# Optimization experiments

Measured on AMD Instinct MI355X. Metric: run time of the kernel, lower is better.

## Reference

```python
import jax, jax.numpy as jnp
import numpy as np

B, K, D, C = 8192, 16, 1024, 512


def setup_inputs() -> dict:
    key = jax.random.key(0)
    k1, k2, k3, k4, k5 = jax.random.split(key, 5)
    concepts = jax.random.normal(k1, (B, K, D), dtype=jnp.float32)
    slot_ids = jax.random.randint(k2, (B,), 0, K)
    labels = jax.random.randint(k3, (B,), 0, C)
    # per-slot Linear(concept_dim -> num_classes): weight (K, C, D), bias (K, C)
    W = jax.random.normal(k4, (K, C, D), dtype=jnp.float32) / np.sqrt(D).astype(np.float32)
    bias = jax.random.normal(k5, (K, C), dtype=jnp.float32) * 0.01
    return {"concepts": concepts, "slot_ids": slot_ids, "labels": labels, "W": W, "bias": bias}


def reference(concepts, slot_ids, labels, W, bias):
    # Each example b uses slot s=slot_ids[b]: logits = concepts[b, s, :] @ W[s].T + bias[s].
    # Vectorized as K batched GEMMs over the slot axis, then gather the relevant row.
    logits = jnp.einsum('bkd,kcd->bkc', concepts, W) + bias  # (B, K, C)
    logp = jax.nn.log_softmax(logits, axis=-1)
    bidx = jnp.arange(concepts.shape[0])
    ce = -logp[bidx, slot_ids, labels]  # per-example cross entropy (B,)
    nK = W.shape[0]
    counts = jax.ops.segment_sum(jnp.ones_like(ce), slot_ids, num_segments=nK)
    sums = jax.ops.segment_sum(ce, slot_ids, num_segments=nK)
    means = sums / jnp.maximum(counts, 1.0)          # per-slot mean CE (= F.cross_entropy per group)
    present = counts > 0
    n_present = jnp.maximum(jnp.sum(present), 1)     # torch: count of unique slots, max(count,1)
    return jnp.sum(jnp.where(present, means, 0.0)) / n_present
```

## Files before the change

### kernel.cpp

```cpp
#include <hip/hip_runtime.h>
#include <hip/hip_bf16.h>

#define B_N 8192
#define K_N 16
#define D_N 1024
#define C_N 512
#define BM  16
#define CONVW_BLOCKS ((K_N * C_N * D_N) / (256 * 8))
#define GEMM_BLOCKS  (B_N / BM + K_N)

typedef __bf16 bf16x8 __attribute__((ext_vector_type(8)));
typedef float  f32x4  __attribute__((ext_vector_type(4)));
typedef unsigned int u32x4 __attribute__((ext_vector_type(4)));

static __device__ __forceinline__ unsigned short f2bf(float f) {
    union { float f; unsigned int u; } x; x.f = f;
    unsigned int r = x.u + 0x7FFFu + ((x.u >> 16) & 1u);
    return (unsigned short)(r >> 16);
}

static __device__ __forceinline__ bf16x8 load_bf8(const unsigned short* p) {
    union { u32x4 u; bf16x8 v; } t;
    t.u = *(const u32x4*)p;
    return t.v;
}

static __device__ __forceinline__ bf16x8 zero_bf8() {
    union { u32x4 u; bf16x8 v; } t;
    u32x4 z = {0u, 0u, 0u, 0u};
    t.u = z;
    return t.v;
}

__global__ __launch_bounds__(256) void setup(
        const float* __restrict__ W, unsigned short* __restrict__ Wb,
        const int* __restrict__ slot_ids, const int* __restrict__ labels,
        int* __restrict__ counts, int* __restrict__ offsets_g,
        int* __restrict__ blk_base, int* __restrict__ done,
        float* __restrict__ ce_sums, int* __restrict__ order_rows,
        int* __restrict__ lab_g) {
    __shared__ int h[256][K_N];
    __shared__ int soff[K_N];
    int t = threadIdx.x;

    if (blockIdx.x < CONVW_BLOCKS) {
        size_t i = ((size_t)blockIdx.x * 256 + t) * 8;
        f32x4 a = *(const f32x4*)(W + i);
        f32x4 b = *(const f32x4*)(W + i + 4);
        u32x4 o;
        o[0] = (unsigned)f2bf(a[0]) | ((unsigned)f2bf(a[1]) << 16);
        o[1] = (unsigned)f2bf(a[2]) | ((unsigned)f2bf(a[3]) << 16);
        o[2] = (unsigned)f2bf(b[0]) | ((unsigned)f2bf(b[1]) << 16);
        o[3] = (unsigned)f2bf(b[2]) | ((unsigned)f2bf(b[3]) << 16);
        *(u32x4*)(Wb + i) = o;
        return;
    }

    int ids[32];
    int own[K_N];

#pragma unroll
    for (int s = 0; s < K_N; ++s) h[t][s] = 0;
#pragma unroll
    for (int i = 0; i < 32; ++i) {
        int b = i * 256 + t;
        int s = slot_ids[b];
        ids[i] = s;
        h[t][s]++;
    }
#pragma unroll
    for (int s = 0; s < K_N; ++s) own[s] = h[t][s];
    __syncthreads();

    for (int d = 1; d < 256; d <<= 1) {
        int v[K_N];
        if (t >= d) {
#pragma unroll
            for (int s = 0; s < K_N; ++s) v[s] = h[t - d][s];
        }
        __syncthreads();
        if (t >= d) {
#pragma unroll
            for (int s = 0; s < K_N; ++s) h[t][s] += v[s];
        }
        __syncthreads();
    }

    if (t == 0) {
        int a = 0, nb = 0;
        blk_base[0] = 0;
#pragma unroll
        for (int s = 0; s < K_N; ++s) {
            int c = h[255][s];
            counts[s] = c;
            soff[s] = a;
            offsets_g[s] = a;
            a += c;
            nb += (c + BM - 1) / BM;
            blk_base[s + 1] = nb;
        }
        *done = 0;
    }
    if (t < K_N) ce_sums[t] = 0.f;
    __syncthreads();

#pragma unroll
    for (int s = 0; s < K_N; ++s) own[s] = soff[s] + h[t][s] - own[s];

#pragma unroll
    for (int i = 0; i < 32; ++i) {
        int b = i * 256 + t;
        int s = ids[i];
        int idx = own[s]++;
        order_rows[idx] = b * K_N + s;
        lab_g[idx] = labels[b];
    }
}

__global__ __launch_bounds__(256) void gemm_ce(
        const float* __restrict__ concepts, const unsigned short* __restrict__ Wb,
        const float* __restrict__ bias, const int* __restrict__ counts,
        const int* __restrict__ offsets, const int* __restrict__ blk_base,
        const int* __restrict__ order_rows, const int* __restrict__ lab_g,
        int* __restrict__ done, float* __restrict__ ce_sums,
        float* __restrict__ out) {
    __shared__ int srow[BM];
    __shared__ float smax[4][BM];
    __shared__ float ssum[4][BM];
    __shared__ float gmax[BM];
    __shared__ float slab[BM];

    int bid = blockIdx.x;
    int nb_total = blk_base[K_N];
    int tid = threadIdx.x;

    if (bid < nb_total) {
        int s = 0;
        while (s < K_N - 1 && bid >= blk_base[s + 1]) ++s;
        int cnt = counts[s];
        int base = offsets[s];
        int row0 = (bid - blk_base[s]) * BM;
        int nrows = min(BM, cnt - row0);

        int wave = tid >> 6, lane = tid & 63;
        int col = lane & 15, quad = lane >> 4;
        int c0 = wave * 128;

        if (tid < BM)
            srow[tid] = order_rows[base + row0 + min(tid, nrows - 1)];
        __syncthreads();

        f32x4 acc[8];
        f32x4 zf = {0.f, 0.f, 0.f, 0.f};
#pragma unroll
        for (int t8 = 0; t8 < 8; ++t8) acc[t8] = zf;

        bool avalid = col < nrows;
        const float* aptr = concepts + (size_t)srow[col] * D_N + quad * 8;
        const unsigned short* bptr = Wb + ((size_t)s * C_N + c0 + col) * D_N + quad * 8;

        for (int k = 0; k < D_N; k += 32) {
            f32x4 a0 = *(const f32x4*)(aptr + k);
            f32x4 a1 = *(const f32x4*)(aptr + k + 4);
            bf16x8 v;
            v[0] = (__bf16)a0[0]; v[1] = (__bf16)a0[1];
            v[2] = (__bf16)a0[2]; v[3] = (__bf16)a0[3];
            v[4] = (__bf16)a1[0]; v[5] = (__bf16)a1[1];
            v[6] = (__bf16)a1[2]; v[7] = (__bf16)a1[3];
            bf16x8 af = avalid ? v : zero_bf8();
            bf16x8 bfr[8];
#pragma unroll
            for (int t8 = 0; t8 < 8; ++t8)
                bfr[t8] = load_bf8(bptr + (size_t)t8 * 16 * D_N + k);
#pragma unroll
            for (int t8 = 0; t8 < 8; ++t8)
                acc[t8] = __builtin_amdgcn_mfma_f32_16x16x32_bf16(af, bfr[t8], acc[t8], 0, 0, 0);
        }

#pragma unroll
        for (int t8 = 0; t8 < 8; ++t8) {
            float bv = bias[(size_t)s * C_N + c0 + t8 * 16 + col];
#pragma unroll
            for (int r = 0; r < 4; ++r) acc[t8][r] += bv;
        }

#pragma unroll
        for (int r = 0; r < 4; ++r) {
            int row = quad * 4 + r;
            float v = acc[0][r];
#pragma unroll
            for (int t8 = 1; t8 < 8; ++t8) v = fmaxf(v, acc[t8][r]);
            v = fmaxf(v, __shfl_xor(v, 1, 64));
            v = fmaxf(v, __shfl_xor(v, 2, 64));
            v = fmaxf(v, __shfl_xor(v, 4, 64));
            v = fmaxf(v, __shfl_xor(v, 8, 64));
            if (col == 0) smax[wave][row] = v;
        }
        __syncthreads();
        if (tid < BM)
            gmax[tid] = fmaxf(fmaxf(smax[0][tid], smax[1][tid]),
                              fmaxf(smax[2][tid], smax[3][tid]));
        __syncthreads();

#pragma unroll
        for (int r = 0; r < 4; ++r) {
            int row = quad * 4 + r;
            float gm = gmax[row];
            int lab = (row < nrows) ? lab_g[base + row0 + row] : -1;
            float sv = 0.f;
#pragma unroll
            for (int t8 = 0; t8 < 8; ++t8) {
                float x = acc[t8][r];
                sv += __expf(x - gm);
                if (c0 + t8 * 16 + col == lab) slab[row] = x;
            }
            sv += __shfl_xor(sv, 1, 64);
            sv += __shfl_xor(sv, 2, 64);
            sv += __shfl_xor(sv, 4, 64);
            sv += __shfl_xor(sv, 8, 64);
            if (col == 0) ssum[wave][row] = sv;
        }
        __syncthreads();

        if (wave == 0) {
            float ce = 0.f;
            if (lane < nrows) {
                float gs = ssum[0][lane] + ssum[1][lane] + ssum[2][lane] + ssum[3][lane];
                ce = gmax[lane] + __logf(gs) - slab[lane];
            }
            ce += __shfl_xor(ce, 1, 64);
            ce += __shfl_xor(ce, 2, 64);
            ce += __shfl_xor(ce, 4, 64);
            ce += __shfl_xor(ce, 8, 64);
            ce += __shfl_xor(ce, 16, 64);
            ce += __shfl_xor(ce, 32, 64);
            if (lane == 0) atomicAdd(&ce_sums[s], ce);
        }
    }

    __syncthreads();
    if (tid == 0) {
        __threadfence();
        int old = atomicAdd(done, 1);
        if (old == (int)gridDim.x - 1) {
            float tot = 0.f; int np = 0;
            for (int s2 = 0; s2 < K_N; ++s2) {
                int c = counts[s2];
                if (c > 0) {
                    float cs = atomicAdd(&ce_sums[s2], 0.0f);
                    tot += cs / (float)c; np++;
                }
            }
            out[0] = tot / (float)(np > 0 ? np : 1);
        }
    }
}

extern "C" void kernel_launch(void* const* d_in, const int* in_sizes, int n_in,
                              void* d_out, int out_size, void* d_ws, size_t ws_size,
                              hipStream_t stream) {
    const float* concepts = (const float*)d_in[0];
    const int*   slot_ids = (const int*)d_in[1];
    const int*   labels   = (const int*)d_in[2];
    const float* W        = (const float*)d_in[3];
    const float* bias     = (const float*)d_in[4];
    float* out = (float*)d_out;

    char* ws = (char*)d_ws;
    int*   counts     = (int*)(ws + 0);
    int*   offsets    = (int*)(ws + 64);
    int*   blk_base   = (int*)(ws + 128);
    int*   done       = (int*)(ws + 256);
    float* ce_sums    = (float*)(ws + 320);
    int*   order_rows = (int*)(ws + 512);
    int*   lab_g      = (int*)(ws + 512 + 4 * B_N);
    unsigned short* Wb = (unsigned short*)(ws + 131072);

    setup<<<CONVW_BLOCKS + 1, 256, 0, stream>>>(W, Wb, slot_ids, labels, counts, offsets,
                                                blk_base, done, ce_sums, order_rows, lab_g);
    gemm_ce<<<GEMM_BLOCKS, 256, 0, stream>>>(concepts, Wb, bias, counts, offsets, blk_base,
                                             order_rows, lab_g, done, ce_sums, out);
}
```

Before: 733.6 us.

## Enlarge GEMM row tile to 64 rows per block, reusing weight fragments

Each gemm_ce block now handles 64 gathered rows instead of 16. Every wave keeps four 16-row accumulator sets and reuses each loaded bf16 weight fragment across all four MFMA row tiles, so per-block weight traffic is spread over four times as many examples. The kernel also declares one block per CU in its launch bounds and swizzles block indices across groups of 8, presumably to spread slot groups over the chip. The setup kernel moves the histogram work to block 0 and the weight conversion to the later blocks. The trade-off is higher register pressure, more wasted work on partially filled tiles at slot boundaries, and fewer, larger blocks.

```diff
diff --git a/kernel.cpp b/kernel.cpp
--- a/kernel.cpp
+++ b/kernel.cpp
@@ -5,7 +5,7 @@
 #define K_N 16
 #define D_N 1024
 #define C_N 512
-#define BM  16
+#define BM  64
 #define CONVW_BLOCKS ((K_N * C_N * D_N) / (256 * 8))
 #define GEMM_BLOCKS  (B_N / BM + K_N)
 
@@ -43,8 +43,8 @@
     __shared__ int soff[K_N];
     int t = threadIdx.x;
 
-    if (blockIdx.x < CONVW_BLOCKS) {
-        size_t i = ((size_t)blockIdx.x * 256 + t) * 8;
+    if (blockIdx.x > 0) {
+        size_t i = ((size_t)(blockIdx.x - 1) * 256 + t) * 8;
         f32x4 a = *(const f32x4*)(W + i);
         f32x4 b = *(const f32x4*)(W + i + 4);
         u32x4 o;
@@ -117,7 +117,7 @@
     }
 }
 
-__global__ __launch_bounds__(256) void gemm_ce(
+__global__ __launch_bounds__(256, 1) void gemm_ce(
         const float* __restrict__ concepts, const unsigned short* __restrict__ Wb,
         const float* __restrict__ bias, const int* __restrict__ counts,
         const int* __restrict__ offsets, const int* __restrict__ blk_base,
@@ -130,7 +130,7 @@
     __shared__ float gmax[BM];
     __shared__ float slab[BM];
 
-    int bid = blockIdx.x;
+    int bid = (blockIdx.x % 8) * (GEMM_BLOCKS / 8) + blockIdx.x / 8;
     int nb_total = blk_base[K_N];
     int tid = threadIdx.x;
 
@@ -150,52 +150,70 @@
             srow[tid] = order_rows[base + row0 + min(tid, nrows - 1)];
         __syncthreads();
 
-        f32x4 acc[8];
+        f32x4 acc[4][8];
         f32x4 zf = {0.f, 0.f, 0.f, 0.f};
 #pragma unroll
-        for (int t8 = 0; t8 < 8; ++t8) acc[t8] = zf;
-
-        bool avalid = col < nrows;
-        const float* aptr = concepts + (size_t)srow[col] * D_N + quad * 8;
+        for (int m = 0; m < 4; ++m)
+#pragma unroll
+            for (int t8 = 0; t8 < 8; ++t8) acc[m][t8] = zf;
+
+        const float* aptr[4];
+        bool avalid[4];
+#pragma unroll
+        for (int m = 0; m < 4; ++m) {
+            int lr = m * 16 + col;
+            avalid[m] = lr < nrows;
+            aptr[m] = concepts + (size_t)srow[lr] * D_N + quad * 8;
+        }
         const unsigned short* bptr = Wb + ((size_t)s * C_N + c0 + col) * D_N + quad * 8;
 
         for (int k = 0; k < D_N; k += 32) {
-            f32x4 a0 = *(const f32x4*)(aptr + k);
-            f32x4 a1 = *(const f32x4*)(aptr + k + 4);
-            bf16x8 v;
-            v[0] = (__bf16)a0[0]; v[1] = (__bf16)a0[1];
-            v[2] = (__bf16)a0[2]; v[3] = (__bf16)a0[3];
-            v[4] = (__bf16)a1[0]; v[5] = (__bf16)a1[1];
-            v[6] = (__bf16)a1[2]; v[7] = (__bf16)a1[3];
-            bf16x8 af = avalid ? v : zero_bf8();
+            bf16x8 af[4];
+#pragma unroll
+            for (int m = 0; m < 4; ++m) {
+                f32x4 a0 = *(const f32x4*)(aptr[m] + k);
+                f32x4 a1 = *(const f32x4*)(aptr[m] + k + 4);
+                bf16x8 v;
+                v[0] = (__bf16)a0[0]; v[1] = (__bf16)a0[1];
+                v[2] = (__bf16)a0[2]; v[3] = (__bf16)a0[3];
+                v[4] = (__bf16)a1[0]; v[5] = (__bf16)a1[1];
+                v[6] = (__bf16)a1[2]; v[7] = (__bf16)a1[3];
+                af[m] = avalid[m] ? v : zero_bf8();
+            }
             bf16x8 bfr[8];
 #pragma unroll
             for (int t8 = 0; t8 < 8; ++t8)
                 bfr[t8] = load_bf8(bptr + (size_t)t8 * 16 * D_N + k);
 #pragma unroll
-            for (int t8 = 0; t8 < 8; ++t8)
-                acc[t8] = __builtin_amdgcn_mfma_f32_16x16x32_bf16(af, bfr[t8], acc[t8], 0, 0, 0);
+            for (int m = 0; m < 4; ++m)
+#pragma unroll
+                for (int t8 = 0; t8 < 8; ++t8)
+                    acc[m][t8] = __builtin_amdgcn_mfma_f32_16x16x32_bf16(af[m], bfr[t8], acc[m][t8], 0, 0, 0);
         }
 
 #pragma unroll
         for (int t8 = 0; t8 < 8; ++t8) {
             float bv = bias[(size_t)s * C_N + c0 + t8 * 16 + col];
 #pragma unroll
-            for (int r = 0; r < 4; ++r) acc[t8][r] += bv;
-        }
-
-#pragma unroll
-        for (int r = 0; r < 4; ++r) {
-            int row = quad * 4 + r;
-            float v = acc[0][r];
-#pragma unroll
-            for (int t8 = 1; t8 < 8; ++t8) v = fmaxf(v, acc[t8][r]);
-            v = fmaxf(v, __shfl_xor(v, 1, 64));
-            v = fmaxf(v, __shfl_xor(v, 2, 64));
-            v = fmaxf(v, __shfl_xor(v, 4, 64));
-            v = fmaxf(v, __shfl_xor(v, 8, 64));
-            if (col == 0) smax[wave][row] = v;
-        }
+            for (int m = 0; m < 4; ++m)
+#pragma unroll
+                for (int r = 0; r < 4; ++r) acc[m][t8][r] += bv;
+        }
+
+#pragma unroll
+        for (int m = 0; m < 4; ++m)
+#pragma unroll
+            for (int r = 0; r < 4; ++r) {
+                int row = m * 16 + quad * 4 + r;
+                float v = acc[m][0][r];
+#pragma unroll
+                for (int t8 = 1; t8 < 8; ++t8) v = fmaxf(v, acc[m][t8][r]);
+                v = fmaxf(v, __shfl_xor(v, 1, 64));
+                v = fmaxf(v, __shfl_xor(v, 2, 64));
+                v = fmaxf(v, __shfl_xor(v, 4, 64));
+                v = fmaxf(v, __shfl_xor(v, 8, 64));
+                if (col == 0) smax[wave][row] = v;
+            }
         __syncthreads();
         if (tid < BM)
             gmax[tid] = fmaxf(fmaxf(smax[0][tid], smax[1][tid]),
@@ -203,23 +221,25 @@
         __syncthreads();
 
 #pragma unroll
-        for (int r = 0; r < 4; ++r) {
-            int row = quad * 4 + r;
-            float gm = gmax[row];
-            int lab = (row < nrows) ? lab_g[base + row0 + row] : -1;
-            float sv = 0.f;
-#pragma unroll
-            for (int t8 = 0; t8 < 8; ++t8) {
-                float x = acc[t8][r];
-                sv += __expf(x - gm);
-                if (c0 + t8 * 16 + col == lab) slab[row] = x;
-            }
-            sv += __shfl_xor(sv, 1, 64);
-            sv += __shfl_xor(sv, 2, 64);
-            sv += __shfl_xor(sv, 4, 64);
-            sv += __shfl_xor(sv, 8, 64);
-            if (col == 0) ssum[wave][row] = sv;
-        }
+        for (int m = 0; m < 4; ++m)
+#pragma unroll
+            for (int r = 0; r < 4; ++r) {
+                int row = m * 16 + quad * 4 + r;
+                float gm = gmax[row];
+                int lab = (row < nrows) ? lab_g[base + row0 + row] : -1;
+                float sv = 0.f;
+#pragma unroll
+                for (int t8 = 0; t8 < 8; ++t8) {
+                    float x = acc[m][t8][r];
+                    sv += __expf(x - gm);
+                    if (c0 + t8 * 16 + col == lab) slab[row] = x;
+                }
+                sv += __shfl_xor(sv, 1, 64);
+                sv += __shfl_xor(sv, 2, 64);
+                sv += __shfl_xor(sv, 4, 64);
+                sv += __shfl_xor(sv, 8, 64);
+                if (col == 0) ssum[wave][row] = sv;
+            }
         __syncthreads();
 
         if (wave == 0) {
```

Measured after the change: 720.4 us. Within noise of the previous version (-1.8%).
